# Kernel tuning notes

Measured on AMD Instinct MI355X. Metric: run time of the kernel, lower is better.

The kernel has to match this reference:

```python
import jax, jax.numpy as jnp
import numpy as np

BLOCKS, LAYERS, KS = 4, 2, 2
DILATIONS = [2 ** i for _ in range(BLOCKS) for i in range(LAYERS)]  # [1,2]*4
B, C_IN, N, T = 16, 2, 2048, 12
RC, DC, SC, EC, OUT = 32, 32, 256, 512, 12
L = BLOCKS * LAYERS
BN_EPS = 1e-5


def setup_inputs() -> dict:
    key = jax.random.key(0)
    ks = jax.random.split(key, 24)
    # raw inputs
    x = jax.random.normal(ks[0], (B, C_IN, N, T), dtype=jnp.float32)
    # two fixed supports: row-normalized random adjacency (dense, as in GraphWaveNet transition matrices)
    A_raw = jax.random.uniform(ks[1], (2, N, N), dtype=jnp.float32)
    A = A_raw / jnp.sum(A_raw, axis=2, keepdims=True)
    nodevec1 = jax.random.normal(ks[2], (N, 10), dtype=jnp.float32)
    nodevec2 = jax.random.normal(ks[3], (10, N), dtype=jnp.float32)
    s = 0.1  # weight scale to keep activations in a sane range
    filter_w = jax.random.normal(ks[4], (L, DC, RC, KS), dtype=jnp.float32) * s
    filter_b = jax.random.normal(ks[5], (L, DC), dtype=jnp.float32) * s
    gate_w = jax.random.normal(ks[6], (L, DC, RC, KS), dtype=jnp.float32) * s
    gate_b = jax.random.normal(ks[7], (L, DC), dtype=jnp.float32) * s
    skip_w = jax.random.normal(ks[8], (L, SC, DC), dtype=jnp.float32) * s
    skip_b = jax.random.normal(ks[9], (L, SC), dtype=jnp.float32) * s
    gcn_w = jax.random.normal(ks[10], (L, RC, 7 * DC), dtype=jnp.float32) * s
    gcn_b = jax.random.normal(ks[11], (L, RC), dtype=jnp.float32) * s
    bn_gamma = 1.0 + 0.1 * jax.random.normal(ks[12], (L, RC), dtype=jnp.float32)
    bn_beta = 0.1 * jax.random.normal(ks[13], (L, RC), dtype=jnp.float32)
    bn_mean = 0.1 * jax.random.normal(ks[14], (L, RC), dtype=jnp.float32)
    bn_var = 1.0 + jax.random.uniform(ks[15], (L, RC), dtype=jnp.float32)
    start_w = jax.random.normal(ks[16], (RC, C_IN), dtype=jnp.float32) * s
    start_b = jax.random.normal(ks[17], (RC,), dtype=jnp.float32) * s
    end1_w = jax.random.normal(ks[18], (EC, SC), dtype=jnp.float32) * s
    end1_b = jax.random.normal(ks[19], (EC,), dtype=jnp.float32) * s
    end2_w = jax.random.normal(ks[20], (OUT, EC), dtype=jnp.float32) * s
    end2_b = jax.random.normal(ks[21], (OUT,), dtype=jnp.float32) * s
    return dict(x=x, A=A, nodevec1=nodevec1, nodevec2=nodevec2,
                filter_w=filter_w, filter_b=filter_b, gate_w=gate_w, gate_b=gate_b,
                skip_w=skip_w, skip_b=skip_b, gcn_w=gcn_w, gcn_b=gcn_b,
                bn_gamma=bn_gamma, bn_beta=bn_beta, bn_mean=bn_mean, bn_var=bn_var,
                start_w=start_w, start_b=start_b, end1_w=end1_w, end1_b=end1_b,
                end2_w=end2_w, end2_b=end2_b)


def _conv1x1(x, w, b):
    # x: [b,c,n,t], w: [o,c] -> [b,o,n,t]
    return jnp.einsum('oc,bcnt->bont', w, x) + b[None, :, None, None]


def _dilated_conv2(x, w, b, d):
    # kernel (1,2) with time dilation d; out length T-d (valid conv)
    xa, xb = x[..., :-d], x[..., d:]
    y = jnp.einsum('oc,bcnt->bont', w[:, :, 0], xa) + jnp.einsum('oc,bcnt->bont', w[:, :, 1], xb)
    return y + b[None, :, None, None]


def _fwd(x, A, nodevec1, nodevec2, filter_w, filter_b, gate_w, gate_b,
         skip_w, skip_b, gcn_w, gcn_b, bn_gamma, bn_beta, bn_mean, bn_var,
         start_w, start_b, end1_w, end1_b, end2_w, end2_b):
    # pad 1 step at the start of time; T becomes 13 == receptive_field
    x = jnp.pad(x, ((0, 0), (0, 0), (0, 0), (1, 0)))
    x = x[:, :2]
    x = _conv1x1(x, start_w, start_b)  # [B,RC,N,13]
    # adaptive adjacency
    adp = jax.nn.softmax(jax.nn.relu(nodevec1 @ nodevec2), axis=1)
    supports = [A[0], A[1], adp]
    skip = None
    for i, d in enumerate(DILATIONS):
        residual = x
        filt = jnp.tanh(_dilated_conv2(residual, filter_w[i], filter_b[i], d))
        gate = jax.nn.sigmoid(_dilated_conv2(residual, gate_w[i], gate_b[i], d))
        x = filt * gate  # [B,DC,N,T-d]
        s = _conv1x1(x, skip_w[i], skip_b[i])  # [B,SC,N,T']
        skip = s if skip is None else s + skip[..., -s.shape[3]:]
        # GCN: order-2 diffusion over 3 supports, concat, 1x1 mix (dropout is identity in eval)
        outs = [x]
        for a in supports:
            x1 = jnp.einsum('bcvt,vw->bcwt', x, a)
            x2 = jnp.einsum('bcvt,vw->bcwt', x1, a)
            outs.extend([x1, x2])
        h = jnp.concatenate(outs, axis=1)  # [B,7*DC,N,T']
        x = _conv1x1(h, gcn_w[i], gcn_b[i])
        x = x + residual[..., -x.shape[3]:]
        # BatchNorm2d in eval mode (running stats)
        inv = bn_gamma[i] / jnp.sqrt(bn_var[i] + BN_EPS)
        x = (x - bn_mean[i][None, :, None, None]) * inv[None, :, None, None] + bn_beta[i][None, :, None, None]
    x = jax.nn.relu(skip)
    x = jax.nn.relu(_conv1x1(x, end1_w, end1_b))
    x = _conv1x1(x, end2_w, end2_b)  # [B,OUT,N,1]
    return x


def reference(x, A, nodevec1, nodevec2, filter_w, filter_b, gate_w, gate_b,
              skip_w, skip_b, gcn_w, gcn_b, bn_gamma, bn_beta, bn_mean, bn_var,
              start_w, start_b, end1_w, end1_b, end2_w, end2_b):
    return _fwd(x, A, nodevec1, nodevec2, filter_w, filter_b, gate_w, gate_b,
                skip_w, skip_b, gcn_w, gcn_b, bn_gamma, bn_beta, bn_mean, bn_var,
                start_w, start_b, end1_w, end1_b, end2_w, end2_b)
```

## Files before the change

### kernel.cpp

```cpp
#include <hip/hip_runtime.h>
#include <math.h>


#define NNODE 2048
#define NLAYER 8
#define SSTR ((size_t)NNODE * NNODE)

typedef unsigned short u16;
typedef __attribute__((ext_vector_type(8))) short bf16x8;
typedef __attribute__((ext_vector_type(4))) float f32x4;

__device__ __forceinline__ u16 f2bf(float f) {
    unsigned u = __builtin_bit_cast(unsigned, f);
    u += 0x7fffu + ((u >> 16) & 1u);
    return (u16)(u >> 16);
}
__device__ __forceinline__ float bf2f(u16 h) {
    unsigned u = ((unsigned)h) << 16;
    return __builtin_bit_cast(float, u);
}

__device__ __forceinline__ void gld16(const void* g, void* l) {
    __builtin_amdgcn_global_load_lds(
        (const __attribute__((address_space(1))) unsigned int*)g,
        (__attribute__((address_space(3))) unsigned int*)l, 16, 0, 0);
}

__global__ __launch_bounds__(256) void k_adp_mm(const float* __restrict__ nv1,
                                                const float* __restrict__ nv2,
                                                float* __restrict__ P) {
    int v = blockIdx.y;
    int w = blockIdx.x * 256 + threadIdx.x;
    float acc = 0.f;
#pragma unroll
    for (int k = 0; k < 10; ++k) acc += nv1[v * 10 + k] * nv2[k * NNODE + w];
    P[(size_t)v * NNODE + w] = acc;
}

__global__ __launch_bounds__(256) void k_softmax(float* __restrict__ P) {
    int v = blockIdx.x, tid = threadIdx.x;
    float* row = P + (size_t)v * NNODE;
    float m = 0.f;
    for (int w = tid; w < NNODE; w += 256) m = fmaxf(m, fmaxf(row[w], 0.f));
#pragma unroll
    for (int off = 32; off > 0; off >>= 1) m = fmaxf(m, __shfl_down(m, off));
    __shared__ float redm[4];
    __shared__ float reds[4];
    int wave = tid >> 6, lane = tid & 63;
    if (lane == 0) redm[wave] = m;
    __syncthreads();
    m = fmaxf(fmaxf(redm[0], redm[1]), fmaxf(redm[2], redm[3]));
    float s = 0.f;
    for (int w = tid; w < NNODE; w += 256) s += expf(fmaxf(row[w], 0.f) - m);
#pragma unroll
    for (int off = 32; off > 0; off >>= 1) s += __shfl_down(s, off);
    if (lane == 0) reds[wave] = s;
    __syncthreads();
    s = reds[0] + reds[1] + reds[2] + reds[3];
    float inv = 1.f / s;
    for (int w = tid; w < NNODE; w += 256) row[w] = expf(fmaxf(row[w], 0.f) - m) * inv;
}

__global__ __launch_bounds__(256) void k_transp(const float* __restrict__ A,
                                                const float* __restrict__ adp,
                                                u16* __restrict__ ST,
                                                u16* __restrict__ Sbf) {
    __shared__ float tile[32][33];
    int s = blockIdx.z;
    const float* src = (s < 2) ? (A + (size_t)s * SSTR) : adp;
    int v0 = blockIdx.y * 32, w0 = blockIdx.x * 32;
    int tx = threadIdx.x & 31, ty = threadIdx.x >> 5;
    u16* dst2 = Sbf + (size_t)s * SSTR;
#pragma unroll
    for (int p = 0; p < 4; ++p) {
        float v = src[(size_t)(v0 + ty + p * 8) * NNODE + w0 + tx];
        tile[ty + p * 8][tx] = v;
        dst2[(size_t)(v0 + ty + p * 8) * NNODE + w0 + tx] = f2bf(v);
    }
    __syncthreads();
    u16* dst = ST + (size_t)(2 * s) * SSTR;
#pragma unroll
    for (int p = 0; p < 4; ++p)
        dst[(size_t)(w0 + ty + p * 8) * NNODE + v0 + tx] = f2bf(tile[tx][ty + p * 8]);
}

__global__ __launch_bounds__(256) void k_gemm_mfma(
    const u16* __restrict__ A, int lda, size_t asstr,
    const u16* __restrict__ BT, size_t bsstr,
    u16* __restrict__ C, int ldc, size_t csstr, int sbase) {
    __shared__ u16 Asl[128 * 32];
    __shared__ u16 Bsl[128 * 32];
    const int tid = threadIdx.x;
    const int wave = tid >> 6, lane = tid & 63;
    const int sidx = sbase + blockIdx.z;
    const u16* Ab = A + sidx * asstr + (size_t)blockIdx.y * 128 * lda;
    const u16* Bb = BT + sidx * bsstr + (size_t)blockIdx.x * 128 * NNODE;
    const int tr = tid >> 2;
    const int tc = (tid & 3) * 8;
    char* AslB = (char*)Asl + wave * 1024;
    char* BslB = (char*)Bsl + wave * 1024;
    const int wm = (wave & 1) * 64, wn = (wave >> 1) * 64;
    const int fr = lane & 15;
    const int fk = (lane >> 4) * 8;
    f32x4 acc[4][4];
#pragma unroll
    for (int i = 0; i < 4; ++i)
#pragma unroll
        for (int j = 0; j < 4; ++j) acc[i][j] = (f32x4){0.f, 0.f, 0.f, 0.f};

    for (int k0 = 0; k0 < 2048; k0 += 32) {
        gld16(Ab + (size_t)tr * lda + k0 + tc, AslB);
        gld16(Ab + (size_t)(tr + 64) * lda + k0 + tc, AslB + 4096);
        gld16(Bb + (size_t)tr * NNODE + k0 + tc, BslB);
        gld16(Bb + (size_t)(tr + 64) * NNODE + k0 + tc, BslB + 4096);
        __syncthreads();
        bf16x8 af[4], bf[4];
#pragma unroll
        for (int i = 0; i < 4; ++i)
            af[i] = *(const bf16x8*)&Asl[(wm + i * 16 + fr) * 32 + fk];
#pragma unroll
        for (int j = 0; j < 4; ++j)
            bf[j] = *(const bf16x8*)&Bsl[(wn + j * 16 + fr) * 32 + fk];
#pragma unroll
        for (int i = 0; i < 4; ++i)
#pragma unroll
            for (int j = 0; j < 4; ++j)
                acc[i][j] = __builtin_amdgcn_mfma_f32_16x16x32_bf16(af[i], bf[j], acc[i][j], 0, 0, 0);
        __syncthreads();
    }
    u16* Cb = C + sidx * csstr + (size_t)(blockIdx.y * 128 + wm) * ldc + blockIdx.x * 128 + wn;
    const int orow = (lane >> 4) * 4;
#pragma unroll
    for (int i = 0; i < 4; ++i)
#pragma unroll
        for (int j = 0; j < 4; ++j)
#pragma unroll
            for (int r = 0; r < 4; ++r)
                Cb[(size_t)(i * 16 + orow + r) * ldc + j * 16 + fr] = f2bf(acc[i][j][r]);
}

__global__ __launch_bounds__(256) void k_gemmZ(const u16* __restrict__ Xg,
                                               const u16* __restrict__ ST,
                                               u16* __restrict__ Z, int pass) {
    __shared__ u16 Asl[128 * 32];
    __shared__ u16 Bsl[128 * 32];
    const int tid = threadIdx.x;
    const int wave = tid >> 6, lane = tid & 63;
    const int m0 = blockIdx.y * 128;
    const int slice = pass * 3 + (blockIdx.x >> 4);
    const int nIn = (blockIdx.x & 15) * 128;
    const u16* Ab = Xg + (size_t)m0 * 2048;
    const u16* Bb = ST + (size_t)slice * SSTR + (size_t)nIn * NNODE;
    const int tr = tid >> 2;
    const int tc = (tid & 3) * 8;
    char* AslB = (char*)Asl + wave * 1024;
    char* BslB = (char*)Bsl + wave * 1024;
    const int wm = (wave & 1) * 64, wn = (wave >> 1) * 64;
    const int fr = lane & 15;
    const int fk = (lane >> 4) * 8;
    f32x4 acc[4][4];
#pragma unroll
    for (int i = 0; i < 4; ++i)
#pragma unroll
        for (int j = 0; j < 4; ++j) acc[i][j] = (f32x4){0.f, 0.f, 0.f, 0.f};

    for (int k0 = 0; k0 < 2048; k0 += 32) {
        gld16(Ab + (size_t)tr * 2048 + k0 + tc, AslB);
        gld16(Ab + (size_t)(tr + 64) * 2048 + k0 + tc, AslB + 4096);
        gld16(Bb + (size_t)tr * NNODE + k0 + tc, BslB);
        gld16(Bb + (size_t)(tr + 64) * NNODE + k0 + tc, BslB + 4096);
        __syncthreads();
        bf16x8 af[4], bf[4];
#pragma unroll
        for (int i = 0; i < 4; ++i)
            af[i] = *(const bf16x8*)&Asl[(wm + i * 16 + fr) * 32 + fk];
#pragma unroll
        for (int j = 0; j < 4; ++j)
            bf[j] = *(const bf16x8*)&Bsl[(wn + j * 16 + fr) * 32 + fk];
#pragma unroll
        for (int i = 0; i < 4; ++i)
#pragma unroll
            for (int j = 0; j < 4; ++j)
                acc[i][j] = __builtin_amdgcn_mfma_f32_16x16x32_bf16(af[i], bf[j], acc[i][j], 0, 0, 0);
        __syncthreads();
    }
    u16* Cb = Z + (size_t)(m0 + wm) * 6144 + blockIdx.x * 128 + wn;
    const int orow = (lane >> 4) * 4;
#pragma unroll
    for (int i = 0; i < 4; ++i)
#pragma unroll
        for (int j = 0; j < 4; ++j)
#pragma unroll
            for (int r = 0; r < 4; ++r)
                Cb[(size_t)(i * 16 + orow + r) * 6144 + j * 16 + fr] = f2bf(acc[i][j][r]);
}

__global__ __launch_bounds__(256) void k_start(const float* __restrict__ xin,
                                               const float* __restrict__ sw,
                                               const float* __restrict__ sb,
                                               u16* __restrict__ out, int b0) {
    int n = blockIdx.x * 256 + threadIdx.x;
    int t = blockIdx.y;
    int bl = blockIdx.z;
    int b = b0 + bl;
    float x0 = 0.f, x1 = 0.f;
    if (t > 0) {
        x0 = xin[((size_t)(b * 2 + 0) * NNODE + n) * 12 + (t - 1)];
        x1 = xin[((size_t)(b * 2 + 1) * NNODE + n) * 12 + (t - 1)];
    }
#pragma unroll
    for (int co = 0; co < 32; ++co) {
        float v = sw[co * 2 + 0] * x0 + sw[co * 2 + 1] * x1 + sb[co];
        out[((size_t)(bl * 32 + co) * 13 + t) * NNODE + n] = f2bf(v);
    }
}

__global__ __launch_bounds__(256) void k_gate(const u16* __restrict__ cur,
                                              u16* __restrict__ xg,
                                              u16* __restrict__ nxt,
                                              int T, int Tn, int d,
                                              const float* __restrict__ fw,
                                              const float* __restrict__ fb,
                                              const float* __restrict__ gw,
                                              const float* __restrict__ gb,
                                              const float* __restrict__ gcwl,
                                              const float* __restrict__ gcbl,
                                              int donxt) {
    __shared__ float4 wp[1024];
    __shared__ float w0[32][33];
    int tid = threadIdx.x;
#pragma unroll
    for (int u = 0; u < 4; ++u) {
        int idx = tid + u * 256;
        int ci = idx >> 5, co = idx & 31;
        wp[idx] = make_float4(fw[co * 64 + ci * 2], fw[co * 64 + ci * 2 + 1],
                              gw[co * 64 + ci * 2], gw[co * 64 + ci * 2 + 1]);
        w0[ci][co] = gcwl[co * 224 + ci];
    }
    __syncthreads();
    int n = blockIdx.x * 512 + tid;
    int t = blockIdx.y;
    int bl = blockIdx.z;
    float f0[32], f1[32], g0[32], g1[32];
#pragma unroll
    for (int co = 0; co < 32; ++co) { f0[co] = 0.f; f1[co] = 0.f; g0[co] = 0.f; g1[co] = 0.f; }
    for (int ci = 0; ci < 32; ++ci) {
        size_t ba = ((size_t)(bl * 32 + ci) * T + t) * NNODE + n;
        size_t bb = ((size_t)(bl * 32 + ci) * T + t + d) * NNODE + n;
        float xa0 = bf2f(cur[ba]), xa1 = bf2f(cur[ba + 256]);
        float xb0 = bf2f(cur[bb]), xb1 = bf2f(cur[bb + 256]);
#pragma unroll
        for (int co = 0; co < 32; ++co) {
            float4 w = wp[ci * 32 + co];
            f0[co] += w.x * xa0 + w.y * xb0;
            f1[co] += w.x * xa1 + w.y * xb1;
            g0[co] += w.z * xa0 + w.w * xb0;
            g1[co] += w.z * xa1 + w.w * xb1;
        }
    }
#pragma unroll
    for (int co = 0; co < 32; ++co) {
        float fbv = fb[co], gbv = gb[co];
        float a0 = tanhf(f0[co] + fbv) * (1.f / (1.f + expf(-(g0[co] + gbv))));
        float a1 = tanhf(f1[co] + fbv) * (1.f / (1.f + expf(-(g1[co] + gbv))));
        f0[co] = a0; f1[co] = a1;
        size_t o = ((size_t)(bl * 32 + co) * Tn + t) * NNODE + n;
        xg[o] = f2bf(a0);
        xg[o + 256] = f2bf(a1);
    }
    if (donxt) {
#pragma unroll
        for (int cop = 0; cop < 32; ++cop) {
            float s0 = gcbl[cop], s1 = s0;
#pragma unroll
            for (int ci = 0; ci < 32; ++ci) {
                float wv = w0[ci][cop];
                s0 += wv * f0[ci];
                s1 += wv * f1[ci];
            }
            size_t o = ((size_t)(bl * 32 + cop) * Tn + t) * NNODE + n;
            nxt[o] = f2bf(s0);
            nxt[o + 256] = f2bf(s1);
        }
    }
}

__global__ __launch_bounds__(256) void k_skip(const u16* __restrict__ xg,
                                              float* __restrict__ skip, int Tn,
                                              const float* __restrict__ sw,
                                              const float* __restrict__ sb, int b0, int init) {
    __shared__ float wl[256];
    int tid = threadIdx.x;
    int sc0 = blockIdx.y * 8;
    wl[tid] = sw[sc0 * 32 + tid];
    __syncthreads();
    int n = blockIdx.x * 256 + tid;
    int bl = blockIdx.z;
    float acc[8];
#pragma unroll
    for (int j = 0; j < 8; ++j) acc[j] = 0.f;
    for (int ci = 0; ci < 32; ci += 4) {
        float v0 = bf2f(xg[((size_t)(bl * 32 + ci + 0) * Tn + (Tn - 1)) * NNODE + n]);
        float v1 = bf2f(xg[((size_t)(bl * 32 + ci + 1) * Tn + (Tn - 1)) * NNODE + n]);
        float v2 = bf2f(xg[((size_t)(bl * 32 + ci + 2) * Tn + (Tn - 1)) * NNODE + n]);
        float v3 = bf2f(xg[((size_t)(bl * 32 + ci + 3) * Tn + (Tn - 1)) * NNODE + n]);
#pragma unroll
        for (int j = 0; j < 8; ++j) {
            float4 w = *(const float4*)&wl[j * 32 + ci];
            acc[j] += w.x * v0 + w.y * v1 + w.z * v2 + w.w * v3;
        }
    }
    int b = b0 + bl;
#pragma unroll
    for (int j = 0; j < 8; ++j) {
        size_t o = ((size_t)(b * 256) + sc0 + j) * NNODE + n;
        float val = acc[j] + sb[sc0 + j];
        if (init) skip[o] = val;
        else skip[o] += val;
    }
}

__global__ __launch_bounds__(256) void k_accum(const u16* __restrict__ Z,
                                               int cbase,
                                               const float* __restrict__ gcnw,
                                               u16* __restrict__ outp,
                                               const u16* __restrict__ resid,
                                               int Tn, int d, int finalf,
                                               const float* __restrict__ bng,
                                               const float* __restrict__ bnb,
                                               const float* __restrict__ bnm,
                                               const float* __restrict__ bnv) {
    __shared__ float wl[3][32][32];
    int tid = threadIdx.x;
    for (int u = tid; u < 3072; u += 256) {
        int g = u >> 10, ci = (u >> 5) & 31, co = u & 31;
        wl[g][ci][co] = gcnw[co * 224 + cbase + g * 32 + ci];
    }
    __syncthreads();
    int n = blockIdx.x * 512 + tid;
    int t = blockIdx.y, bl = blockIdx.z;
    float a0[32], a1[32];
#pragma unroll
    for (int co = 0; co < 32; ++co) { a0[co] = 0.f; a1[co] = 0.f; }
    for (int ci = 0; ci < 32; ++ci) {
        size_t m = (size_t)(bl * 32 + ci) * Tn + t;
#pragma unroll
        for (int g = 0; g < 3; ++g) {
            float v0 = bf2f(Z[m * 6144 + g * 2048 + n]);
            float v1 = bf2f(Z[m * 6144 + g * 2048 + n + 256]);
#pragma unroll
            for (int cq = 0; cq < 8; ++cq) {
                float4 w = *(const float4*)&wl[g][ci][cq * 4];
                a0[cq * 4 + 0] += w.x * v0; a1[cq * 4 + 0] += w.x * v1;
                a0[cq * 4 + 1] += w.y * v0; a1[cq * 4 + 1] += w.y * v1;
                a0[cq * 4 + 2] += w.z * v0; a1[cq * 4 + 2] += w.z * v1;
                a0[cq * 4 + 3] += w.w * v0; a1[cq * 4 + 3] += w.w * v1;
            }
        }
    }
#pragma unroll
    for (int co = 0; co < 32; ++co) {
        size_t o = ((size_t)(bl * 32 + co) * Tn + t) * NNODE + n;
        float v0 = bf2f(outp[o]) + a0[co];
        float v1 = bf2f(outp[o + 256]) + a1[co];
        if (finalf) {
            size_t ro = ((size_t)(bl * 32 + co) * (Tn + d) + t + d) * NNODE + n;
            v0 += bf2f(resid[ro]); v1 += bf2f(resid[ro + 256]);
            float inv = bng[co] * rsqrtf(bnv[co] + 1e-5f);
            float mu = bnm[co], be = bnb[co];
            v0 = (v0 - mu) * inv + be;
            v1 = (v1 - mu) * inv + be;
        }
        outp[o] = f2bf(v0); outp[o + 256] = f2bf(v1);
    }
}

__global__ __launch_bounds__(256) void k_skipT(const float* __restrict__ skip,
                                               u16* __restrict__ skipT) {
    __shared__ float tile[32][33];
    int b = blockIdx.z;
    int n0 = blockIdx.x * 32, c0 = blockIdx.y * 32;
    int tx = threadIdx.x & 31, ty = threadIdx.x >> 5;
#pragma unroll
    for (int p = 0; p < 4; ++p)
        tile[ty + p * 8][tx] = skip[((size_t)b * 256 + c0 + ty + p * 8) * NNODE + n0 + tx];
    __syncthreads();
#pragma unroll
    for (int p = 0; p < 4; ++p)
        skipT[((size_t)b * NNODE + n0 + ty + p * 8) * 256 + c0 + tx] =
            f2bf(fmaxf(tile[tx][ty + p * 8], 0.f));
}

__global__ __launch_bounds__(256) void k_cast(const float* __restrict__ src,
                                              u16* __restrict__ dst) {
    int i = blockIdx.x * 256 + threadIdx.x;
    dst[i] = f2bf(src[i]);
}

__global__ __launch_bounds__(256) void k_end1m(const u16* __restrict__ E1,
                                               const u16* __restrict__ skT,
                                               const float* __restrict__ bias,
                                               u16* __restrict__ h) {
    __shared__ u16 Asl[128 * 32];
    __shared__ u16 Bsl[128 * 32];
    const int tid = threadIdx.x;
    const int wave = tid >> 6, lane = tid & 63;
    const int b = blockIdx.z;
    const int m0 = blockIdx.y * 128;
    const int n0 = blockIdx.x * 128;
    const int tr = tid >> 2;
    const int tc = (tid & 3) * 8;
    char* AslB = (char*)Asl + wave * 1024;
    char* BslB = (char*)Bsl + wave * 1024;
    const int wm = (wave & 1) * 64, wn = (wave >> 1) * 64;
    const int fr = lane & 15;
    const int fk = (lane >> 4) * 8;
    const u16* Ab = E1 + (size_t)m0 * 256;
    const u16* Bb = skT + ((size_t)b * NNODE + n0) * 256;
    f32x4 acc[4][4];
#pragma unroll
    for (int i = 0; i < 4; ++i)
#pragma unroll
        for (int j = 0; j < 4; ++j) acc[i][j] = (f32x4){0.f, 0.f, 0.f, 0.f};
    for (int k0 = 0; k0 < 256; k0 += 32) {
        gld16(Ab + (size_t)tr * 256 + k0 + tc, AslB);
        gld16(Ab + (size_t)(tr + 64) * 256 + k0 + tc, AslB + 4096);
        gld16(Bb + (size_t)tr * 256 + k0 + tc, BslB);
        gld16(Bb + (size_t)(tr + 64) * 256 + k0 + tc, BslB + 4096);
        __syncthreads();
        bf16x8 af[4], bf[4];
#pragma unroll
        for (int i = 0; i < 4; ++i)
            af[i] = *(const bf16x8*)&Asl[(wm + i * 16 + fr) * 32 + fk];
#pragma unroll
        for (int j = 0; j < 4; ++j)
            bf[j] = *(const bf16x8*)&Bsl[(wn + j * 16 + fr) * 32 + fk];
#pragma unroll
        for (int i = 0; i < 4; ++i)
#pragma unroll
            for (int j = 0; j < 4; ++j)
                acc[i][j] = __builtin_amdgcn_mfma_f32_16x16x32_bf16(af[i], bf[j], acc[i][j], 0, 0, 0);
        __syncthreads();
    }
    const int orow = (lane >> 4) * 4;
#pragma unroll
    for (int i = 0; i < 4; ++i)
#pragma unroll
        for (int r = 0; r < 4; ++r) {
            int m = m0 + wm + i * 16 + orow + r;
            float bs = bias[m];
            size_t ob = ((size_t)b * 512 + m) * NNODE + n0 + wn;
#pragma unroll
            for (int j = 0; j < 4; ++j)
                h[ob + j * 16 + fr] = f2bf(fmaxf(acc[i][j][r] + bs, 0.f));
        }
}

__global__ __launch_bounds__(256) void k_end2(const u16* __restrict__ h,
                                              const float* __restrict__ w,
                                              const float* __restrict__ bias,
                                              float* __restrict__ out) {
    __shared__ float wl[512];
    int tid = threadIdx.x;
    int o = blockIdx.y;
    wl[tid] = w[o * 512 + tid];
    wl[tid + 256] = w[o * 512 + tid + 256];
    __syncthreads();
    int n = blockIdx.x * 256 + tid;
    int b = blockIdx.z;
    float acc = 0.f;
    for (int e = 0; e < 512; ++e) acc += wl[e] * bf2f(h[((size_t)(b * 512) + e) * NNODE + n]);
    out[((size_t)(b * 12) + o) * NNODE + n] = acc + bias[o];
}

extern "C" void kernel_launch(void* const* d_in, const int* in_sizes, int n_in,
                              void* d_out, int out_size, void* d_ws, size_t ws_size,
                              hipStream_t stream) {
    const float* x_in = (const float*)d_in[0];
    const float* A    = (const float*)d_in[1];
    const float* nv1  = (const float*)d_in[2];
    const float* nv2  = (const float*)d_in[3];
    const float* fw   = (const float*)d_in[4];
    const float* fb   = (const float*)d_in[5];
    const float* gw   = (const float*)d_in[6];
    const float* gb   = (const float*)d_in[7];
    const float* skw  = (const float*)d_in[8];
    const float* skb  = (const float*)d_in[9];
    const float* gcw  = (const float*)d_in[10];
    const float* gcb  = (const float*)d_in[11];
    const float* bng  = (const float*)d_in[12];
    const float* bnb  = (const float*)d_in[13];
    const float* bnm  = (const float*)d_in[14];
    const float* bnv  = (const float*)d_in[15];
    const float* stw  = (const float*)d_in[16];
    const float* stb  = (const float*)d_in[17];
    const float* e1w  = (const float*)d_in[18];
    const float* e1b  = (const float*)d_in[19];
    const float* e2w  = (const float*)d_in[20];
    const float* e2b  = (const float*)d_in[21];
    (void)in_sizes; (void)n_in; (void)out_size;

    const int BL = (ws_size >= 239075328UL) ? 16 : 8;
    const int nch = 16 / BL;
    const size_t bufsz = (size_t)BL * 1703936UL;

    char* base = (char*)d_ws;
    u16*   ST   = (u16*)base;
    float* skip = (float*)(base + 50331648UL);
    u16*   bufA = (u16*)(base + 83886080UL);
    u16*   bufB = (u16*)(base + 83886080UL + bufsz);
    u16*   xg   = (u16*)(base + 83886080UL + 2 * bufsz);
    u16*   Z    = (u16*)(base + 83886080UL + 2 * bufsz + (size_t)BL * 1572864UL);
    float* adp  = (float*)Z;
    u16*   Sbf  = (u16*)bufA;
    u16*   h     = (u16*)(base + 83886080UL);
    u16*   skipT = (u16*)(base + 83886080UL + 33554432UL);
    u16*   E1bf  = (u16*)ST;

    k_adp_mm<<<dim3(8, 2048), 256, 0, stream>>>(nv1, nv2, adp);
    k_softmax<<<2048, 256, 0, stream>>>(adp);
    k_transp<<<dim3(64, 64, 3), 256, 0, stream>>>(A, adp, ST, Sbf);
    k_gemm_mfma<<<dim3(16, 16, 3), 256, 0, stream>>>(
        ST, NNODE, 2 * SSTR, Sbf, SSTR, ST + SSTR, NNODE, 2 * SSTR, 0);

    static const int DIL[NLAYER] = {1, 2, 1, 2, 1, 2, 1, 2};
    for (int ch = 0; ch < nch; ++ch) {
        int b0 = ch * BL;
        k_start<<<dim3(8, 13, BL), 256, 0, stream>>>(x_in, stw, stb, bufA, b0);
        u16* cur = bufA;
        u16* nxt = bufB;
        int T = 13;
        for (int i = 0; i < NLAYER; ++i) {
            int d = DIL[i], Tn = T - d;
            int last = (i == NLAYER - 1);
            k_gate<<<dim3(4, Tn, BL), 256, 0, stream>>>(cur, xg, nxt, T, Tn, d,
                fw + i * 2048, fb + i * 32, gw + i * 2048, gb + i * 32,
                gcw + i * 32 * 224, gcb + i * 32, last ? 0 : 1);
            k_skip<<<dim3(8, 32, BL), 256, 0, stream>>>(xg, skip, Tn,
                skw + i * 256 * 32, skb + i * 256, b0, (i == 0) ? 1 : 0);
            if (last) break;
            int MB = BL * Tn / 4;
            const float* gcwi = gcw + i * 32 * 224;
            for (int p = 0; p < 2; ++p) {
                k_gemmZ<<<dim3(48, MB), 256, 0, stream>>>(xg, ST, Z, p);
                k_accum<<<dim3(4, Tn, BL), 256, 0, stream>>>(
                    Z, 32 + 96 * p, gcwi, nxt, cur, Tn, d, p,
                    bng + i * 32, bnb + i * 32, bnm + i * 32, bnv + i * 32);
            }
            u16* tmp = cur; cur = nxt; nxt = tmp;
            T = Tn;
        }
    }
    k_cast<<<512, 256, 0, stream>>>(e1w, E1bf);
    k_skipT<<<dim3(64, 8, 16), 256, 0, stream>>>(skip, skipT);
    k_end1m<<<dim3(16, 4, 16), 256, 0, stream>>>(E1bf, skipT, e1b, h);
    k_end2<<<dim3(8, 12, 16), 256, 0, stream>>>(h, e2w, e2b, (float*)d_out);
}
```

Measured before the change: 3.361 ms.

## Vectorize bf16 pair accesses, swap gemmZ grid order, fuse end2 outputs

The gate, skip and accum kernels now load and store adjacent node pairs as packed 32-bit words, where before each thread handled two nodes 256 apart with separate 16-bit accesses. The skip kernel's grid is halved to match. The Z GEMM grid is transposed so consecutive blocks share the same activation tile and walk across support columns, which changes cache reuse order. The final end2 kernel computes all 12 outputs per thread from a single read of h instead of re-reading h once per output channel.

```diff
diff --git a/kernel.cpp b/kernel.cpp
--- a/kernel.cpp
+++ b/kernel.cpp
@@ -7,6 +7,7 @@
 #define SSTR ((size_t)NNODE * NNODE)
 
 typedef unsigned short u16;
+typedef unsigned int u32;
 typedef __attribute__((ext_vector_type(8))) short bf16x8;
 typedef __attribute__((ext_vector_type(4))) float f32x4;
 
@@ -18,6 +19,11 @@
 __device__ __forceinline__ float bf2f(u16 h) {
     unsigned u = ((unsigned)h) << 16;
     return __builtin_bit_cast(float, u);
+}
+__device__ __forceinline__ float bflo(u32 p) { return __builtin_bit_cast(float, p << 16); }
+__device__ __forceinline__ float bfhi(u32 p) { return __builtin_bit_cast(float, p & 0xffff0000u); }
+__device__ __forceinline__ u32 pack2(float a, float b) {
+    return (u32)f2bf(a) | ((u32)f2bf(b) << 16);
 }
 
 __device__ __forceinline__ void gld16(const void* g, void* l) {
@@ -146,9 +152,10 @@
     __shared__ u16 Bsl[128 * 32];
     const int tid = threadIdx.x;
     const int wave = tid >> 6, lane = tid & 63;
-    const int m0 = blockIdx.y * 128;
-    const int slice = pass * 3 + (blockIdx.x >> 4);
-    const int nIn = (blockIdx.x & 15) * 128;
+    const int m0 = blockIdx.x * 128;
+    const int sl = blockIdx.y >> 4;
+    const int nIn = (blockIdx.y & 15) * 128;
+    const int slice = pass * 3 + sl;
     const u16* Ab = Xg + (size_t)m0 * 2048;
     const u16* Bb = ST + (size_t)slice * SSTR + (size_t)nIn * NNODE;
     const int tr = tid >> 2;
@@ -184,7 +191,7 @@
                 acc[i][j] = __builtin_amdgcn_mfma_f32_16x16x32_bf16(af[i], bf[j], acc[i][j], 0, 0, 0);
         __syncthreads();
     }
-    u16* Cb = Z + (size_t)(m0 + wm) * 6144 + blockIdx.x * 128 + wn;
+    u16* Cb = Z + (size_t)(m0 + wm) * 6144 + sl * 2048 + nIn + wn;
     const int orow = (lane >> 4) * 4;
 #pragma unroll
     for (int i = 0; i < 4; ++i)
@@ -238,7 +245,7 @@
         w0[ci][co] = gcwl[co * 224 + ci];
     }
     __syncthreads();
-    int n = blockIdx.x * 512 + tid;
+    int n = blockIdx.x * 512 + tid * 2;
     int t = blockIdx.y;
     int bl = blockIdx.z;
     float f0[32], f1[32], g0[32], g1[32];
@@ -247,8 +254,10 @@
     for (int ci = 0; ci < 32; ++ci) {
         size_t ba = ((size_t)(bl * 32 + ci) * T + t) * NNODE + n;
         size_t bb = ((size_t)(bl * 32 + ci) * T + t + d) * NNODE + n;
-        float xa0 = bf2f(cur[ba]), xa1 = bf2f(cur[ba + 256]);
-        float xb0 = bf2f(cur[bb]), xb1 = bf2f(cur[bb + 256]);
+        u32 ua = *(const u32*)&cur[ba];
+        u32 ub = *(const u32*)&cur[bb];
+        float xa0 = bflo(ua), xa1 = bfhi(ua);
+        float xb0 = bflo(ub), xb1 = bfhi(ub);
 #pragma unroll
         for (int co = 0; co < 32; ++co) {
             float4 w = wp[ci * 32 + co];
@@ -265,8 +274,7 @@
         float a1 = tanhf(f1[co] + fbv) * (1.f / (1.f + expf(-(g1[co] + gbv))));
         f0[co] = a0; f1[co] = a1;
         size_t o = ((size_t)(bl * 32 + co) * Tn + t) * NNODE + n;
-        xg[o] = f2bf(a0);
-        xg[o + 256] = f2bf(a1);
+        *(u32*)&xg[o] = pack2(a0, a1);
     }
     if (donxt) {
 #pragma unroll
@@ -279,8 +287,7 @@
                 s1 += wv * f1[ci];
             }
             size_t o = ((size_t)(bl * 32 + cop) * Tn + t) * NNODE + n;
-            nxt[o] = f2bf(s0);
-            nxt[o + 256] = f2bf(s1);
+            *(u32*)&nxt[o] = pack2(s0, s1);
         }
     }
 }
@@ -294,29 +301,34 @@
     int sc0 = blockIdx.y * 8;
     wl[tid] = sw[sc0 * 32 + tid];
     __syncthreads();
-    int n = blockIdx.x * 256 + tid;
+    int n = blockIdx.x * 512 + tid * 2;
     int bl = blockIdx.z;
-    float acc[8];
-#pragma unroll
-    for (int j = 0; j < 8; ++j) acc[j] = 0.f;
-    for (int ci = 0; ci < 32; ci += 4) {
-        float v0 = bf2f(xg[((size_t)(bl * 32 + ci + 0) * Tn + (Tn - 1)) * NNODE + n]);
-        float v1 = bf2f(xg[((size_t)(bl * 32 + ci + 1) * Tn + (Tn - 1)) * NNODE + n]);
-        float v2 = bf2f(xg[((size_t)(bl * 32 + ci + 2) * Tn + (Tn - 1)) * NNODE + n]);
-        float v3 = bf2f(xg[((size_t)(bl * 32 + ci + 3) * Tn + (Tn - 1)) * NNODE + n]);
+    float a0[8], a1[8];
+#pragma unroll
+    for (int j = 0; j < 8; ++j) { a0[j] = 0.f; a1[j] = 0.f; }
+    for (int ci = 0; ci < 32; ci += 2) {
+        u32 p0 = *(const u32*)&xg[((size_t)(bl * 32 + ci + 0) * Tn + (Tn - 1)) * NNODE + n];
+        u32 p1 = *(const u32*)&xg[((size_t)(bl * 32 + ci + 1) * Tn + (Tn - 1)) * NNODE + n];
+        float v00 = bflo(p0), v01 = bfhi(p0);
+        float v10 = bflo(p1), v11 = bfhi(p1);
 #pragma unroll
         for (int j = 0; j < 8; ++j) {
-            float4 w = *(const float4*)&wl[j * 32 + ci];
-            acc[j] += w.x * v0 + w.y * v1 + w.z * v2 + w.w * v3;
+            float wA = wl[j * 32 + ci], wB = wl[j * 32 + ci + 1];
+            a0[j] += wA * v00 + wB * v10;
+            a1[j] += wA * v01 + wB * v11;
         }
     }
     int b = b0 + bl;
 #pragma unroll
     for (int j = 0; j < 8; ++j) {
         size_t o = ((size_t)(b * 256) + sc0 + j) * NNODE + n;
-        float val = acc[j] + sb[sc0 + j];
-        if (init) skip[o] = val;
-        else skip[o] += val;
+        float bsv = sb[sc0 + j];
+        if (init) {
+            *(float2*)&skip[o] = make_float2(a0[j] + bsv, a1[j] + bsv);
+        } else {
+            float2 old = *(const float2*)&skip[o];
+            *(float2*)&skip[o] = make_float2(old.x + a0[j] + bsv, old.y + a1[j] + bsv);
+        }
     }
 }
 
@@ -337,7 +349,7 @@
         wl[g][ci][co] = gcnw[co * 224 + cbase + g * 32 + ci];
     }
     __syncthreads();
-    int n = blockIdx.x * 512 + tid;
+    int n = blockIdx.x * 512 + tid * 2;
     int t = blockIdx.y, bl = blockIdx.z;
     float a0[32], a1[32];
 #pragma unroll
@@ -346,8 +358,8 @@
         size_t m = (size_t)(bl * 32 + ci) * Tn + t;
 #pragma unroll
         for (int g = 0; g < 3; ++g) {
-            float v0 = bf2f(Z[m * 6144 + g * 2048 + n]);
-            float v1 = bf2f(Z[m * 6144 + g * 2048 + n + 256]);
+            u32 zz = *(const u32*)&Z[m * 6144 + g * 2048 + n];
+            float v0 = bflo(zz), v1 = bfhi(zz);
 #pragma unroll
             for (int cq = 0; cq < 8; ++cq) {
                 float4 w = *(const float4*)&wl[g][ci][cq * 4];
@@ -361,17 +373,19 @@
 #pragma unroll
     for (int co = 0; co < 32; ++co) {
         size_t o = ((size_t)(bl * 32 + co) * Tn + t) * NNODE + n;
-        float v0 = bf2f(outp[o]) + a0[co];
-        float v1 = bf2f(outp[o + 256]) + a1[co];
+        u32 oo = *(const u32*)&outp[o];
+        float v0 = bflo(oo) + a0[co];
+        float v1 = bfhi(oo) + a1[co];
         if (finalf) {
             size_t ro = ((size_t)(bl * 32 + co) * (Tn + d) + t + d) * NNODE + n;
-            v0 += bf2f(resid[ro]); v1 += bf2f(resid[ro + 256]);
+            u32 rr = *(const u32*)&resid[ro];
+            v0 += bflo(rr); v1 += bfhi(rr);
             float inv = bng[co] * rsqrtf(bnv[co] + 1e-5f);
             float mu = bnm[co], be = bnb[co];
             v0 = (v0 - mu) * inv + be;
             v1 = (v1 - mu) * inv + be;
         }
-        outp[o] = f2bf(v0); outp[o + 256] = f2bf(v1);
+        *(u32*)&outp[o] = pack2(v0, v1);
     }
 }
 
@@ -460,17 +474,24 @@
                                               const float* __restrict__ w,
                                               const float* __restrict__ bias,
                                               float* __restrict__ out) {
-    __shared__ float wl[512];
+    __shared__ float wl[12][512];
     int tid = threadIdx.x;
-    int o = blockIdx.y;
-    wl[tid] = w[o * 512 + tid];
-    wl[tid + 256] = w[o * 512 + tid + 256];
+    for (int u = tid; u < 6144; u += 256) wl[u >> 9][u & 511] = w[u];
     __syncthreads();
     int n = blockIdx.x * 256 + tid;
-    int b = blockIdx.z;
-    float acc = 0.f;
-    for (int e = 0; e < 512; ++e) acc += wl[e] * bf2f(h[((size_t)(b * 512) + e) * NNODE + n]);
-    out[((size_t)(b * 12) + o) * NNODE + n] = acc + bias[o];
+    int b = blockIdx.y;
+    float acc[12];
+#pragma unroll
+    for (int o = 0; o < 12; ++o) acc[o] = 0.f;
+#pragma unroll 4
+    for (int e = 0; e < 512; ++e) {
+        float v = bf2f(h[((size_t)(b * 512) + e) * NNODE + n]);
+#pragma unroll
+        for (int o = 0; o < 12; ++o) acc[o] += wl[o][e] * v;
+    }
+#pragma unroll
+    for (int o = 0; o < 12; ++o)
+        out[((size_t)(b * 12) + o) * NNODE + n] = acc[o] + bias[o];
 }
 
 extern "C" void kernel_launch(void* const* d_in, const int* in_sizes, int n_in,
@@ -536,13 +557,13 @@
             k_gate<<<dim3(4, Tn, BL), 256, 0, stream>>>(cur, xg, nxt, T, Tn, d,
                 fw + i * 2048, fb + i * 32, gw + i * 2048, gb + i * 32,
                 gcw + i * 32 * 224, gcb + i * 32, last ? 0 : 1);
-            k_skip<<<dim3(8, 32, BL), 256, 0, stream>>>(xg, skip, Tn,
+            k_skip<<<dim3(4, 32, BL), 256, 0, stream>>>(xg, skip, Tn,
                 skw + i * 256 * 32, skb + i * 256, b0, (i == 0) ? 1 : 0);
             if (last) break;
             int MB = BL * Tn / 4;
             const float* gcwi = gcw + i * 32 * 224;
             for (int p = 0; p < 2; ++p) {
-                k_gemmZ<<<dim3(48, MB), 256, 0, stream>>>(xg, ST, Z, p);
+                k_gemmZ<<<dim3(MB, 48), 256, 0, stream>>>(xg, ST, Z, p);
                 k_accum<<<dim3(4, Tn, BL), 256, 0, stream>>>(
                     Z, 32 + 96 * p, gcwi, nxt, cur, Tn, d, p,
                     bng + i * 32, bnb + i * 32, bnm + i * 32, bnv + i * 32);
@@ -554,5 +575,5 @@
     k_cast<<<512, 256, 0, stream>>>(e1w, E1bf);
     k_skipT<<<dim3(64, 8, 16), 256, 0, stream>>>(skip, skipT);
     k_end1m<<<dim3(16, 4, 16), 256, 0, stream>>>(E1bf, skipT, e1b, h);
-    k_end2<<<dim3(8, 12, 16), 256, 0, stream>>>(h, e2w, e2b, (float*)d_out);
-}
+    k_end2<<<dim3(8, 16), 256, 0, stream>>>(h, e2w, e2b, (float*)d_out);
+}
```

Result: no change. 3.381 ms (+0.6%).
